# Performance work log

Hardware: AMD Instinct MI355X
Metric: run time of the kernel (lower is better)

## Reference

```python
import jax, jax.numpy as jnp
import numpy as np

B, N, NUM = 16384, 512, 3  # batch, num queries, num vanishing points per image


def setup_inputs() -> dict:
    key = jax.random.key(0)
    k1, k2, k3 = jax.random.split(key, 3)
    pred_logits = jax.random.normal(k1, (B, N, 1), jnp.float32)
    pp = jax.random.normal(k2, (B, N, 3), jnp.float32)
    pred_pos = pp / jnp.linalg.norm(pp, axis=-1, keepdims=True)  # unit directions
    vp = jax.random.normal(k3, (B, 3, NUM), jnp.float32)
    vps_unique = vp / jnp.linalg.norm(vp, axis=1, keepdims=True)  # all columns valid (abs-sum > 1e-5)
    return {"pred_logits": pred_logits, "pred_pos": pred_pos, "vps_unique": vps_unique}


def _greedy_select(conf, pos, num):
    # conf: [N,1], pos: [N,3]; greedy angular NMS keeping `num` candidates.
    order = jnp.argsort(-conf[:, 0]).astype(jnp.int32)  # descending confidence
    thresh = jnp.pi / (num + 1)
    ar = jnp.arange(num)
    cand0 = jnp.zeros((num,), jnp.int32).at[0].set(order[0])

    def step(carry, idx):
        cand, count = carry
        sel = pos[cand]                                   # [num,3]
        dots = jnp.minimum(jnp.abs(sel @ pos[idx]), 1.0)  # clip for arccos stability
        ang = jnp.where(ar < count, jnp.arccos(dots), jnp.inf)
        add = (count < num) & (jnp.min(ang) >= thresh)    # torch: skip if dst < pi/(num+1)
        cand = jnp.where(add & (ar == count), idx, cand)
        return (cand, count + add.astype(jnp.int32)), None

    (cand, _), _ = jax.lax.scan(step, (cand0, jnp.int32(1)), order[1:])
    return pos[cand]  # [num,3]


def reference(pred_logits, pred_pos, vps_unique):
    num = vps_unique.shape[2]  # static: all vps columns are valid by construction
    sel = jax.vmap(lambda c, p: _greedy_select(c, p, num))(pred_logits, pred_pos)
    return sel  # [B, num, 3]
```

## Files before the change

### kernel.cpp

```cpp
#include <hip/hip_runtime.h>
#include <math.h>

#define B_TOTAL 16384
#define NQ 512
#define NUM 3

__global__ __launch_bounds__(256) void greedy_nms_kernel(
    const float* __restrict__ conf,
    const float* __restrict__ pos,
    float* __restrict__ out)
{
    const int wave = threadIdx.x >> 6;
    const int lane = threadIdx.x & 63;
    const int b = (blockIdx.x << 2) + wave;

    const float* cb = conf + (size_t)b * NQ;
    const float* pb = pos  + (size_t)b * NQ * 3;

    const float4* cb4 = reinterpret_cast<const float4*>(cb);
    float4 u0 = cb4[lane * 2 + 0];
    float4 u1 = cb4[lane * 2 + 1];
    float fv[8] = {u0.x, u0.y, u0.z, u0.w, u1.x, u1.y, u1.z, u1.w};

    unsigned k[8];
    #pragma unroll
    for (int s = 0; s < 8; ++s) {
        int bi = __float_as_int(fv[s]);
        k[s] = (unsigned)bi ^ ((unsigned)(bi >> 31) | 0x80000000u);
    }

    auto next_winner = [&]() -> int {
        unsigned m01 = k[0]; int i01 = 0; if (k[1] > m01) { m01 = k[1]; i01 = 1; }
        unsigned m23 = k[2]; int i23 = 2; if (k[3] > m23) { m23 = k[3]; i23 = 3; }
        unsigned m45 = k[4]; int i45 = 4; if (k[5] > m45) { m45 = k[5]; i45 = 5; }
        unsigned m67 = k[6]; int i67 = 6; if (k[7] > m67) { m67 = k[7]; i67 = 7; }
        if (m23 > m01) { m01 = m23; i01 = i23; }
        if (m67 > m45) { m45 = m67; i45 = i67; }
        if (m45 > m01) { m01 = m45; i01 = i45; }
        unsigned long long key =
            ((unsigned long long)m01 << 32) |
            (unsigned)(NQ - 1 - ((lane << 3) + i01));
        #pragma unroll
        for (int off = 32; off > 0; off >>= 1) {
            unsigned long long o = __shfl_xor(key, off);
            if (o > key) key = o;
        }
        int n = NQ - 1 - (int)(unsigned)key;
        if ((n >> 3) == lane) {
            const int sl = n & 7;
            #pragma unroll
            for (int s = 0; s < 8; ++s)
                if (sl == s) k[s] = 0u;
        }
        return n;
    };

    const float TH  = 0.78539816339744830961f;
    const float CLO = 0.70710478f;
    const float CHI = 0.70710878f;

    float a0x = 0.f, a0y = 0.f, a0z = 0.f;
    float a1x = 0.f, a1y = 0.f, a1z = 0.f;
    float a2x = 0.f, a2y = 0.f, a2z = 0.f;
    int count = 0;

    #pragma unroll 1
    for (int t = 0; t < NQ; ++t) {
        const int n = next_winner();
        const float px = pb[n * 3 + 0];
        const float py = pb[n * 3 + 1];
        const float pz = pb[n * 3 + 2];

        const float d0 = fabsf(a0x * px + a0y * py + a0z * pz);
        const float d1 = fabsf(a1x * px + a1y * py + a1z * pz);
        const float d2 = fabsf(a2x * px + a2y * py + a2z * pz);
        const float dm = fmaxf(d0, fmaxf(d1, d2));

        bool add;
        if (dm <= CLO) {
            add = true;
        } else if (dm >= CHI) {
            add = false;
        } else {
            add = (acosf(fminf(d0, 1.f)) >= TH) &&
                  (acosf(fminf(d1, 1.f)) >= TH) &&
                  (acosf(fminf(d2, 1.f)) >= TH);
        }

        if (add) {
            if (count == 0)      { a0x = px; a0y = py; a0z = pz; }
            else if (count == 1) { a1x = px; a1y = py; a1z = pz; }
            else                 { a2x = px; a2y = py; a2z = pz; }
            if (++count == NUM) break;
        }
    }

    if (count < NUM) {
        float p0x = pb[0], p0y = pb[1], p0z = pb[2];
        if (count == 0) { a0x = p0x; a0y = p0y; a0z = p0z; }
        if (count <= 1) { a1x = p0x; a1y = p0y; a1z = p0z; }
        a2x = p0x; a2y = p0y; a2z = p0z;
    }

    if (lane == 0) {
        float* ob = out + (size_t)b * 9;
        ob[0] = a0x; ob[1] = a0y; ob[2] = a0z;
        ob[3] = a1x; ob[4] = a1y; ob[5] = a1z;
        ob[6] = a2x; ob[7] = a2y; ob[8] = a2z;
    }
}

extern "C" void kernel_launch(void* const* d_in, const int* in_sizes, int n_in,
                              void* d_out, int out_size, void* d_ws, size_t ws_size,
                              hipStream_t stream) {
    const float* pred_logits = (const float*)d_in[0];
    const float* pred_pos    = (const float*)d_in[1];
    float* out = (float*)d_out;

    const int grid = B_TOTAL / 4;
    greedy_nms_kernel<<<grid, 256, 0, stream>>>(pred_logits, pred_pos, out);
}
```

Measured before the change: 29.13 us.

## Process four batches per wave with 16-lane groups and wider per-thread argmax

Each wave now handles four images, with one 16-lane group per image. Each lane holds 32 confidence keys instead of 8, so the per-step argmax needs a deeper in-register tree but only four shuffle rounds instead of six. The loop exits only when all groups in the wave have selected three candidates, via a wave-wide vote. This trades more register work and divergence across groups for fewer waves and fewer cross-lane reductions per image.

```diff
diff --git a/kernel.cpp b/kernel.cpp
--- a/kernel.cpp
+++ b/kernel.cpp
@@ -10,48 +10,56 @@
     const float* __restrict__ pos,
     float* __restrict__ out)
 {
-    const int wave = threadIdx.x >> 6;
-    const int lane = threadIdx.x & 63;
-    const int b = (blockIdx.x << 2) + wave;
+    const int gid = threadIdx.x >> 4;
+    const int t   = threadIdx.x & 15;
+    const int b   = (blockIdx.x << 4) + gid;
 
     const float* cb = conf + (size_t)b * NQ;
     const float* pb = pos  + (size_t)b * NQ * 3;
 
+    unsigned k[32];
     const float4* cb4 = reinterpret_cast<const float4*>(cb);
-    float4 u0 = cb4[lane * 2 + 0];
-    float4 u1 = cb4[lane * 2 + 1];
-    float fv[8] = {u0.x, u0.y, u0.z, u0.w, u1.x, u1.y, u1.z, u1.w};
-
-    unsigned k[8];
     #pragma unroll
-    for (int s = 0; s < 8; ++s) {
-        int bi = __float_as_int(fv[s]);
-        k[s] = (unsigned)bi ^ ((unsigned)(bi >> 31) | 0x80000000u);
+    for (int j = 0; j < 8; ++j) {
+        float4 u = cb4[j * 16 + t];
+        float f[4] = {u.x, u.y, u.z, u.w};
+        #pragma unroll
+        for (int c = 0; c < 4; ++c) {
+            int bi = __float_as_int(f[c]);
+            k[j * 4 + c] = (unsigned)bi ^ ((unsigned)(bi >> 31) | 0x80000000u);
+        }
     }
 
     auto next_winner = [&]() -> int {
-        unsigned m01 = k[0]; int i01 = 0; if (k[1] > m01) { m01 = k[1]; i01 = 1; }
-        unsigned m23 = k[2]; int i23 = 2; if (k[3] > m23) { m23 = k[3]; i23 = 3; }
-        unsigned m45 = k[4]; int i45 = 4; if (k[5] > m45) { m45 = k[5]; i45 = 5; }
-        unsigned m67 = k[6]; int i67 = 6; if (k[7] > m67) { m67 = k[7]; i67 = 7; }
-        if (m23 > m01) { m01 = m23; i01 = i23; }
-        if (m67 > m45) { m45 = m67; i45 = i67; }
-        if (m45 > m01) { m01 = m45; i01 = i45; }
+        unsigned mv[16]; int ms[16];
+        #pragma unroll
+        for (int i = 0; i < 16; ++i) {
+            bool sel = k[2 * i + 1] > k[2 * i];
+            mv[i] = sel ? k[2 * i + 1] : k[2 * i];
+            ms[i] = sel ? (2 * i + 1) : (2 * i);
+        }
+        #pragma unroll
+        for (int st = 8; st >= 1; st >>= 1) {
+            #pragma unroll
+            for (int i = 0; i < st; ++i)
+                if (mv[i + st] > mv[i]) {
+                    mv[i] = mv[i + st]; ms[i] = ms[i + st];
+                }
+        }
+        const int nl = ((ms[0] >> 2) << 6) | (t << 2) | (ms[0] & 3);
         unsigned long long key =
-            ((unsigned long long)m01 << 32) |
-            (unsigned)(NQ - 1 - ((lane << 3) + i01));
+            ((unsigned long long)mv[0] << 32) | (unsigned)(NQ - 1 - nl);
         #pragma unroll
-        for (int off = 32; off > 0; off >>= 1) {
+        for (int off = 1; off <= 8; off <<= 1) {
             unsigned long long o = __shfl_xor(key, off);
             if (o > key) key = o;
         }
-        int n = NQ - 1 - (int)(unsigned)key;
-        if ((n >> 3) == lane) {
-            const int sl = n & 7;
-            #pragma unroll
-            for (int s = 0; s < 8; ++s)
-                if (sl == s) k[s] = 0u;
-        }
+        const int n = NQ - 1 - (int)(unsigned)key;
+        const int owner = (n >> 2) & 15;
+        const int slx = (owner == t) ? (((n >> 6) << 2) | (n & 3)) : 64;
+        #pragma unroll
+        for (int s = 0; s < 32; ++s)
+            if (slx == s) k[s] = 0u;
         return n;
     };
 
@@ -65,7 +73,7 @@
     int count = 0;
 
     #pragma unroll 1
-    for (int t = 0; t < NQ; ++t) {
+    for (int it = 0; it < NQ; ++it) {
         const int n = next_winner();
         const float px = pb[n * 3 + 0];
         const float py = pb[n * 3 + 1];
@@ -87,12 +95,13 @@
                   (acosf(fminf(d2, 1.f)) >= TH);
         }
 
-        if (add) {
+        if (add && count < NUM) {
             if (count == 0)      { a0x = px; a0y = py; a0z = pz; }
             else if (count == 1) { a1x = px; a1y = py; a1z = pz; }
             else                 { a2x = px; a2y = py; a2z = pz; }
-            if (++count == NUM) break;
+            ++count;
         }
+        if (__all(count >= NUM)) break;
     }
 
     if (count < NUM) {
@@ -102,7 +111,7 @@
         a2x = p0x; a2y = p0y; a2z = p0z;
     }
 
-    if (lane == 0) {
+    if (t == 0) {
         float* ob = out + (size_t)b * 9;
         ob[0] = a0x; ob[1] = a0y; ob[2] = a0z;
         ob[3] = a1x; ob[4] = a1y; ob[5] = a1z;
@@ -117,6 +126,6 @@
     const float* pred_pos    = (const float*)d_in[1];
     float* out = (float*)d_out;
 
-    const int grid = B_TOTAL / 4;
+    const int grid = B_TOTAL / 16;
     greedy_nms_kernel<<<grid, 256, 0, stream>>>(pred_logits, pred_pos, out);
 }
```

Result: slower. 38.54 us (+32.3%).
